# Kernel optimization log

Measured on AMD Instinct MI355X. Metric: run time of the kernel, lower is better.

## Reference

```python
import jax, jax.numpy as jnp
import numpy as np


def _ce(logits, labels):
    # per-element cross entropy; logits [N,C], labels [N] int
    logp = jax.nn.log_softmax(logits, axis=-1)
    return -jnp.take_along_axis(logp, labels[:, None].astype(jnp.int32), axis=1)[:, 0]


def _masked_mean(x, m):
    cnt = jnp.sum(m)
    return jnp.where(cnt > 0, jnp.sum(x * m) / jnp.maximum(cnt, 1.0), 0.0)


def _ohem(predict, target, train_mask, negative_ratio=3.0):
    # predict [N,2], target/train_mask [N] int {0,1}
    pos = (target * train_mask) > 0
    neg = ((1 - target) * train_mask) > 0
    n_pos = jnp.sum(pos).astype(jnp.float32)
    loss_all = _ce(predict, target)
    loss_pos = jnp.where(n_pos > 0, jnp.sum(jnp.where(pos, loss_all, 0.0)), 0.0)
    n_neg_total = jnp.sum(neg)
    n_neg = jnp.where(n_pos > 0,
                      jnp.minimum(n_neg_total, (negative_ratio * n_pos).astype(jnp.int32)),
                      jnp.minimum(100, n_neg_total))
    # hard-negative mining: top-n_neg of the per-pixel negative CE losses
    neg_sorted = jnp.sort(jnp.where(neg, loss_all, -jnp.inf))[::-1]
    loss_neg = jnp.sum(jnp.where(jnp.arange(neg_sorted.shape[0]) < n_neg, neg_sorted, 0.0))
    return (loss_pos + loss_neg) / (n_pos + n_neg.astype(jnp.float32))


def _forward(inputs, gcn_pred, gcn_labels, train_mask, tr_mask, tcl_mask, radii_map, sin_map, cos_map):
    B, C, H, W = inputs.shape
    ch = jnp.transpose(inputs, (0, 2, 3, 1)).reshape(-1, C)  # [N,8], N=B*H*W
    tr_pred = ch[:, 0:2]
    tcl_pred = ch[:, 2:4]
    sin_pred = ch[:, 4]
    cos_pred = ch[:, 5]
    scale = jnp.sqrt(1.0 / (sin_pred ** 2 + cos_pred ** 2 + 1e-4))
    sin_pred = sin_pred * scale
    cos_pred = cos_pred * scale
    top_pred = ch[:, 6]
    bot_pred = ch[:, 7]

    tm = train_mask.reshape(-1)
    tr = tr_mask.reshape(-1)
    tcl = tcl_mask[:, :, :, 0].reshape(-1)
    sin_t = sin_map.reshape(-1)
    cos_t = cos_map.reshape(-1)
    top_t = radii_map[:, :, :, 0].reshape(-1)
    bot_t = radii_map[:, :, :, 1].reshape(-1)

    # TR loss with OHEM hard-negative mining
    loss_tr = _ohem(tr_pred, tr, tm)

    # TCL loss: mean CE over train_mask*tr_mask positives
    tr_train = ((tm * tr) > 0).astype(jnp.float32)
    loss_tcl = _masked_mean(_ce(tcl_pred, tcl), tr_train)

    # geometry losses over tcl_mask pixels
    tclm = (tcl > 0).astype(jnp.float32)
    d_top = jnp.abs(top_pred / (top_t + 0.01) - 1.0)
    d_bot = jnp.abs(bot_pred / (bot_t + 0.01) - 1.0)
    sl_top = jnp.where(d_top < 1.0, 0.5 * d_top * d_top, d_top - 0.5)  # torch smooth_l1 (beta=1)
    sl_bot = jnp.where(d_bot < 1.0, 0.5 * d_bot * d_bot, d_bot - 0.5)
    loss_radii = _masked_mean(sl_top + sl_bot, tclm)

    sigma = 9.0
    d_sin = jnp.abs(sin_pred - sin_t)
    d_cos = jnp.abs(cos_pred - cos_t)
    sl_sin = jnp.where(d_sin < 1.0 / sigma, 0.5 * d_sin * d_sin * sigma, d_sin - 0.5 / sigma)
    sl_cos = jnp.where(d_cos < 1.0 / sigma, 0.5 * d_cos * d_cos * sigma, d_cos - 0.5 / sigma)
    loss_sin = _masked_mean(sl_sin, tclm)
    loss_cos = _masked_mean(sl_cos, tclm)

    gcn_loss = jnp.mean(_ce(gcn_pred, gcn_labels.reshape(-1)))
    return (loss_tr, loss_tcl, loss_sin, loss_cos, loss_radii, gcn_loss)


def setup_inputs() -> dict:
    key = jax.random.key(0)
    ks = jax.random.split(key, 9)
    B, H, W = 8, 640, 640
    return {
        'inputs': jax.random.normal(ks[0], (B, 8, H, W), dtype=jnp.float32),
        'gcn_pred': jax.random.normal(ks[1], (4096, 2), dtype=jnp.float32),
        'gcn_labels': jax.random.randint(ks[2], (4096,), 0, 2, dtype=jnp.int32),
        'train_mask': jax.random.randint(ks[3], (B, H, W), 0, 2, dtype=jnp.int32),
        'tr_mask': jax.random.randint(ks[4], (B, H, W), 0, 2, dtype=jnp.int32),
        'tcl_mask': jax.random.randint(ks[5], (B, H, W, 2), 0, 2, dtype=jnp.int32),
        'radii_map': jax.random.uniform(ks[6], (B, H, W, 2), dtype=jnp.float32),
        'sin_map': jax.random.normal(ks[7], (B, H, W), dtype=jnp.float32),
        'cos_map': jax.random.normal(ks[8], (B, H, W), dtype=jnp.float32),
    }


def reference(inputs, gcn_pred, gcn_labels, train_mask, tr_mask, tcl_mask, radii_map, sin_map, cos_map):
    return _forward(inputs, gcn_pred, gcn_labels, train_mask, tr_mask, tcl_mask, radii_map, sin_map, cos_map)
```

## Files before the change

### kernel.cpp

```cpp
#include <hip/hip_runtime.h>

#define HW_ 409600
#define NPIX 3276800
#define NB 4096
#define NGCN 4096
#define NBLK 1600

struct Ws {
  double sums[8];
  unsigned int cnts[8];
  unsigned int hcnt[NB];
  float hsum[NB];
  float pf[NBLK][8];
  unsigned int pc[NBLK][4];
};

__device__ __forceinline__ float ce2(float a0, float a1, int label) {
  float mx = fmaxf(a0, a1);
  float mn = fminf(a0, a1);
  float lse = mx + __logf(1.0f + __expf(mn - mx));
  return lse - (label ? a1 : a0);
}

struct Acc {
  float s_pos, s_neg, s_tcl, s_sin, s_cos, s_rad;
  unsigned int c_pos, c_neg, c_tcl;
  float mx_neg;
};

struct Pack {
  float4 v0, v1, v2, v3, v4, v5, v6, v7;
  int4 wtm, wtr, tca, tcb;
  float4 ra, rb, vs, vc;

  __device__ __forceinline__ void load(
      int g, const float* __restrict__ inp, const int* __restrict__ tmm,
      const int* __restrict__ trm, const int* __restrict__ tclm,
      const float* __restrict__ radm, const float* __restrict__ sinm,
      const float* __restrict__ cosm) {
    int p = g * 4;
    int b = p / HW_;
    int q = p - b * HW_;
    const float* base = inp + (size_t)b * 8 * HW_ + q;
    v0 = *(const float4*)(base);
    v1 = *(const float4*)(base + HW_);
    v2 = *(const float4*)(base + 2 * HW_);
    v3 = *(const float4*)(base + 3 * HW_);
    v4 = *(const float4*)(base + 4 * HW_);
    v5 = *(const float4*)(base + 5 * HW_);
    v6 = *(const float4*)(base + 6 * HW_);
    v7 = *(const float4*)(base + 7 * HW_);
    wtm = *(const int4*)(tmm + p);
    wtr = *(const int4*)(trm + p);
    tca = *(const int4*)(tclm + 2 * p);
    tcb = *(const int4*)(tclm + 2 * p + 4);
    ra = *(const float4*)(radm + 2 * p);
    rb = *(const float4*)(radm + 2 * p + 4);
    vs = *(const float4*)(sinm + p);
    vc = *(const float4*)(cosm + p);
  }

  __device__ __forceinline__ void compute(Acc& a) {
    float a0[4] = {v0.x, v0.y, v0.z, v0.w};
    float a1[4] = {v1.x, v1.y, v1.z, v1.w};
    float a2[4] = {v2.x, v2.y, v2.z, v2.w};
    float a3[4] = {v3.x, v3.y, v3.z, v3.w};
    float a4[4] = {v4.x, v4.y, v4.z, v4.w};
    float a5[4] = {v5.x, v5.y, v5.z, v5.w};
    float a6[4] = {v6.x, v6.y, v6.z, v6.w};
    float a7[4] = {v7.x, v7.y, v7.z, v7.w};
    int tmj[4] = {wtm.x, wtm.y, wtm.z, wtm.w};
    int trj[4] = {wtr.x, wtr.y, wtr.z, wtr.w};
    int tcj[4] = {tca.x, tca.z, tcb.x, tcb.z};
    float topt[4] = {ra.x, ra.z, rb.x, rb.z};
    float bott[4] = {ra.y, ra.w, rb.y, rb.w};
    float sint[4] = {vs.x, vs.y, vs.z, vs.w};
    float cost[4] = {vc.x, vc.y, vc.z, vc.w};
#pragma unroll
    for (int j = 0; j < 4; ++j) {
      bool pos = (trj[j] * tmj[j]) > 0;
      bool neg = ((1 - trj[j]) * tmj[j]) > 0;
      float ltr = ce2(a0[j], a1[j], trj[j]);
      if (pos) { a.s_pos += ltr; a.c_pos++; }
      if (neg) { a.s_neg += ltr; a.c_neg++; a.mx_neg = fmaxf(a.mx_neg, ltr); }
      float ltc = ce2(a2[j], a3[j], tcj[j]);
      if (pos) a.s_tcl += ltc;
      bool tc = tcj[j] > 0;
      float sp = a4[j], cp = a5[j];
      float sc = __builtin_amdgcn_rsqf(sp * sp + cp * cp + 1e-4f);
      sp *= sc; cp *= sc;
      float dsin = fabsf(sp - sint[j]);
      float dcos = fabsf(cp - cost[j]);
      const float inv9 = 1.f / 9.f;
      float slsin = dsin < inv9 ? 4.5f * dsin * dsin : dsin - 0.5f * inv9;
      float slcos = dcos < inv9 ? 4.5f * dcos * dcos : dcos - 0.5f * inv9;
      float dtop = fabsf(a6[j] * __builtin_amdgcn_rcpf(topt[j] + 0.01f) - 1.f);
      float dbot = fabsf(a7[j] * __builtin_amdgcn_rcpf(bott[j] + 0.01f) - 1.f);
      float sltop = dtop < 1.f ? 0.5f * dtop * dtop : dtop - 0.5f;
      float slbot = dbot < 1.f ? 0.5f * dbot * dbot : dbot - 0.5f;
      if (tc) { a.s_sin += slsin; a.s_cos += slcos; a.s_rad += sltop + slbot; a.c_tcl++; }
    }
  }
};

__global__ __launch_bounds__(256, 4) void k_main(
    const float* __restrict__ inp,
    const float* __restrict__ gcn_pred,
    const int* __restrict__ gcn_lab,
    const int* __restrict__ tmm,
    const int* __restrict__ trm,
    const int* __restrict__ tclm,
    const float* __restrict__ radm,
    const float* __restrict__ sinm,
    const float* __restrict__ cosm,
    Ws* __restrict__ ws) {
  Acc a = {0.f, 0.f, 0.f, 0.f, 0.f, 0.f, 0u, 0u, 0u, 0.f};
  float s_gcn = 0.f;

  int tid = threadIdx.x + blockIdx.x * blockDim.x;

  if (tid < NGCN) {
    s_gcn = ce2(gcn_pred[2 * tid], gcn_pred[2 * tid + 1], gcn_lab[tid]);
  }

  Pack A, B;
  A.load(tid,          inp, tmm, trm, tclm, radm, sinm, cosm);
  B.load(tid + 409600, inp, tmm, trm, tclm, radm, sinm, cosm);
  A.compute(a);
  B.compute(a);

#pragma unroll
  for (int off = 32; off > 0; off >>= 1) {
    a.s_pos += __shfl_down(a.s_pos, off);
    a.s_neg += __shfl_down(a.s_neg, off);
    a.s_tcl += __shfl_down(a.s_tcl, off);
    a.s_sin += __shfl_down(a.s_sin, off);
    a.s_cos += __shfl_down(a.s_cos, off);
    a.s_rad += __shfl_down(a.s_rad, off);
    s_gcn   += __shfl_down(s_gcn, off);
    a.c_pos += __shfl_down(a.c_pos, off);
    a.c_neg += __shfl_down(a.c_neg, off);
    a.c_tcl += __shfl_down(a.c_tcl, off);
    a.mx_neg = fmaxf(a.mx_neg, __shfl_down(a.mx_neg, off));
  }
  __shared__ float shf[4][8];
  __shared__ unsigned int shc[4][3];
  int wv = threadIdx.x >> 6, ln = threadIdx.x & 63;
  if (ln == 0) {
    shf[wv][0] = a.s_pos; shf[wv][1] = a.s_neg; shf[wv][2] = a.s_tcl; shf[wv][3] = a.s_sin;
    shf[wv][4] = a.s_cos; shf[wv][5] = a.s_rad; shf[wv][6] = s_gcn;  shf[wv][7] = a.mx_neg;
    shc[wv][0] = a.c_pos; shc[wv][1] = a.c_neg; shc[wv][2] = a.c_tcl;
  }
  __syncthreads();
  if (threadIdx.x == 0) {
    float f0 = 0, f1 = 0, f2 = 0, f3 = 0, f4 = 0, f5 = 0, f6 = 0, f7 = 0;
    unsigned int u0 = 0, u1 = 0, u2 = 0;
#pragma unroll
    for (int w = 0; w < 4; ++w) {
      f0 += shf[w][0]; f1 += shf[w][1]; f2 += shf[w][2]; f3 += shf[w][3];
      f4 += shf[w][4]; f5 += shf[w][5]; f6 += shf[w][6];
      f7 = fmaxf(f7, shf[w][7]);
      u0 += shc[w][0]; u1 += shc[w][1]; u2 += shc[w][2];
    }
    ws->pf[blockIdx.x][0] = f0; ws->pf[blockIdx.x][1] = f1;
    ws->pf[blockIdx.x][2] = f2; ws->pf[blockIdx.x][3] = f3;
    ws->pf[blockIdx.x][4] = f4; ws->pf[blockIdx.x][5] = f5;
    ws->pf[blockIdx.x][6] = f6; ws->pf[blockIdx.x][7] = f7;
    ws->pc[blockIdx.x][0] = u0; ws->pc[blockIdx.x][1] = u1; ws->pc[blockIdx.x][2] = u2;
  }
}

__global__ __launch_bounds__(1024) void k_reduce(Ws* __restrict__ ws, float* __restrict__ out) {
  int t = threadIdx.x;
#pragma unroll
  for (int i = t; i < NB; i += 1024) { ws->hcnt[i] = 0u; ws->hsum[i] = 0.f; }

  float f[8] = {0, 0, 0, 0, 0, 0, 0, 0};
  unsigned int u[3] = {0, 0, 0};
#pragma unroll
  for (int rep = 0; rep < 2; ++rep) {
    int s = t + rep * 1024;
    if (s < NBLK) {
#pragma unroll
      for (int i = 0; i < 7; ++i) f[i] += ws->pf[s][i];
      f[7] = fmaxf(f[7], ws->pf[s][7]);
#pragma unroll
      for (int i = 0; i < 3; ++i) u[i] += ws->pc[s][i];
    }
  }
#pragma unroll
  for (int off = 32; off > 0; off >>= 1) {
#pragma unroll
    for (int i = 0; i < 7; ++i) f[i] += __shfl_down(f[i], off);
    f[7] = fmaxf(f[7], __shfl_down(f[7], off));
#pragma unroll
    for (int i = 0; i < 3; ++i) u[i] += __shfl_down(u[i], off);
  }
  __shared__ float shf[16][8];
  __shared__ unsigned int shc[16][3];
  int wv = t >> 6, ln = t & 63;
  if (ln == 0) {
#pragma unroll
    for (int i = 0; i < 8; ++i) shf[wv][i] = f[i];
#pragma unroll
    for (int i = 0; i < 3; ++i) shc[wv][i] = u[i];
  }
  __syncthreads();
  if (t == 0) {
    double d[7] = {0, 0, 0, 0, 0, 0, 0};
    float mx = 0.f;
    unsigned int np = 0, nnt = 0, ntc = 0;
#pragma unroll
    for (int w = 0; w < 16; ++w) {
#pragma unroll
      for (int i = 0; i < 7; ++i) d[i] += (double)shf[w][i];
      mx = fmaxf(mx, shf[w][7]);
      np += shc[w][0]; nnt += shc[w][1]; ntc += shc[w][2];
    }
    ws->sums[0] = d[0];
    ws->cnts[0] = np;
    ws->cnts[5] = __float_as_uint(mx);
    out[1] = np > 0 ? (float)(d[2] / (double)np) : 0.f;
    out[2] = ntc > 0 ? (float)(d[3] / (double)ntc) : 0.f;
    out[3] = ntc > 0 ? (float)(d[4] / (double)ntc) : 0.f;
    out[4] = ntc > 0 ? (float)(d[5] / (double)ntc) : 0.f;
    out[5] = (float)(d[6] / (double)NGCN);
    long long nneg;
    if (np > 0) {
      long long cap = (long long)(int)(3.0f * (float)np);
      nneg = (long long)nnt < cap ? (long long)nnt : cap;
    } else {
      nneg = (long long)nnt < 100 ? (long long)nnt : 100;
    }
    if (nneg >= (long long)nnt) {
      out[0] = (float)((d[0] + d[1]) / ((double)np + (double)nneg));
      ws->cnts[3] = 0u;
    } else {
      ws->cnts[3] = 1u;
      ws->cnts[4] = (unsigned int)nneg;
    }
  }
}

__global__ __launch_bounds__(256) void k_hist(
    const float* __restrict__ inp,
    const int* __restrict__ tmm,
    const int* __restrict__ trm,
    Ws* __restrict__ ws) {
  if (ws->cnts[3] == 0u) return;
  __shared__ unsigned int lc[NB];
  __shared__ float lsum[NB];
  for (int i = threadIdx.x; i < NB; i += blockDim.x) { lc[i] = 0u; lsum[i] = 0.f; }
  __syncthreads();
  float maxneg = __uint_as_float(ws->cnts[5]);
  float invmax = maxneg > 0.f ? (float)NB / maxneg : 0.f;
  int tid = threadIdx.x + blockIdx.x * blockDim.x;
  int nth = blockDim.x * gridDim.x;
  for (int p = tid; p < NPIX; p += nth) {
    int tmj = tmm[p], trj = trm[p];
    if (((1 - trj) * tmj) > 0) {
      int b = p / HW_;
      int q = p - b * HW_;
      const float* base = inp + (size_t)b * 8 * HW_ + q;
      float ltr = ce2(base[0], base[HW_], trj);
      int bin = (int)(ltr * invmax);
      bin = bin < NB - 1 ? bin : NB - 1;
      bin = bin > 0 ? bin : 0;
      atomicAdd(&lc[bin], 1u);
      atomicAdd(&lsum[bin], ltr);
    }
  }
  __syncthreads();
  for (int i = threadIdx.x; i < NB; i += blockDim.x) {
    if (lc[i]) {
      atomicAdd(&ws->hcnt[i], lc[i]);
      atomicAdd(&ws->hsum[i], lsum[i]);
    }
  }
}

__global__ void k_fin2(Ws* __restrict__ ws, float* __restrict__ out) {
  if (threadIdx.x != 0 || blockIdx.x != 0) return;
  if (ws->cnts[3] == 0u) return;
  unsigned int k = ws->cnts[4];
  double acc = 0.0;
  unsigned int cum = 0;
  for (int b = NB - 1; b >= 0 && cum < k; --b) {
    unsigned int c = ws->hcnt[b];
    if (!c) continue;
    float s = ws->hsum[b];
    if (cum + c <= k) {
      acc += (double)s;
      cum += c;
    } else {
      unsigned int r = k - cum;
      acc += (double)r * ((double)s / (double)c);
      cum = k;
    }
  }
  unsigned int np = ws->cnts[0];
  double spos = ws->sums[0];
  out[0] = (float)((spos + acc) / ((double)np + (double)k));
}

extern "C" void kernel_launch(void* const* d_in, const int* in_sizes, int n_in,
                              void* d_out, int out_size, void* d_ws, size_t ws_size,
                              hipStream_t stream) {
  (void)in_sizes; (void)n_in; (void)out_size; (void)ws_size;
  const float* inp = (const float*)d_in[0];
  const float* gcn_pred = (const float*)d_in[1];
  const int* gcn_lab = (const int*)d_in[2];
  const int* tmm = (const int*)d_in[3];
  const int* trm = (const int*)d_in[4];
  const int* tclm = (const int*)d_in[5];
  const float* radm = (const float*)d_in[6];
  const float* sinm = (const float*)d_in[7];
  const float* cosm = (const float*)d_in[8];
  float* out = (float*)d_out;
  Ws* ws = (Ws*)d_ws;

  k_main<<<NBLK, 256, 0, stream>>>(inp, gcn_pred, gcn_lab, tmm, trm, tclm, radm, sinm, cosm, ws);
  k_reduce<<<1, 1024, 0, stream>>>(ws, out);
  k_hist<<<256, 256, 0, stream>>>(inp, tmm, trm, ws);
  k_fin2<<<1, 64, 0, stream>>>(ws, out);
}
```

Baseline: 54.99 us.

## Interleave dual-pack loads, fold final top-k pass into histogram kernel

The main kernel now issues all loads for both pixel groups up front, interleaved, before any compute. Its occupancy hint drops from 4 to 2 blocks per SM to leave room for the extra live registers. The separate single-thread finalisation kernel is removed: the last histogram block, found with an atomic counter that is reset in the reduce kernel, now does the top-k walk. The histogram grid shrinks from 256 to 64 blocks, which saves a launch but gives each block more pixels to process in that pass.

New measurement: 48.01 us. 1.15x faster.

```diff
diff --git a/kernel.cpp b/kernel.cpp
--- a/kernel.cpp
+++ b/kernel.cpp
@@ -5,6 +5,10 @@
 #define NB 4096
 #define NGCN 4096
 #define NBLK 1600
+#define HBLK 64
+
+typedef float vf4 __attribute__((ext_vector_type(4)));
+typedef int vi4 __attribute__((ext_vector_type(4)));
 
 struct Ws {
   double sums[8];
@@ -28,82 +32,51 @@
   float mx_neg;
 };
 
-struct Pack {
-  float4 v0, v1, v2, v3, v4, v5, v6, v7;
-  int4 wtm, wtr, tca, tcb;
-  float4 ra, rb, vs, vc;
-
-  __device__ __forceinline__ void load(
-      int g, const float* __restrict__ inp, const int* __restrict__ tmm,
-      const int* __restrict__ trm, const int* __restrict__ tclm,
-      const float* __restrict__ radm, const float* __restrict__ sinm,
-      const float* __restrict__ cosm) {
-    int p = g * 4;
-    int b = p / HW_;
-    int q = p - b * HW_;
-    const float* base = inp + (size_t)b * 8 * HW_ + q;
-    v0 = *(const float4*)(base);
-    v1 = *(const float4*)(base + HW_);
-    v2 = *(const float4*)(base + 2 * HW_);
-    v3 = *(const float4*)(base + 3 * HW_);
-    v4 = *(const float4*)(base + 4 * HW_);
-    v5 = *(const float4*)(base + 5 * HW_);
-    v6 = *(const float4*)(base + 6 * HW_);
-    v7 = *(const float4*)(base + 7 * HW_);
-    wtm = *(const int4*)(tmm + p);
-    wtr = *(const int4*)(trm + p);
-    tca = *(const int4*)(tclm + 2 * p);
-    tcb = *(const int4*)(tclm + 2 * p + 4);
-    ra = *(const float4*)(radm + 2 * p);
-    rb = *(const float4*)(radm + 2 * p + 4);
-    vs = *(const float4*)(sinm + p);
-    vc = *(const float4*)(cosm + p);
-  }
-
-  __device__ __forceinline__ void compute(Acc& a) {
-    float a0[4] = {v0.x, v0.y, v0.z, v0.w};
-    float a1[4] = {v1.x, v1.y, v1.z, v1.w};
-    float a2[4] = {v2.x, v2.y, v2.z, v2.w};
-    float a3[4] = {v3.x, v3.y, v3.z, v3.w};
-    float a4[4] = {v4.x, v4.y, v4.z, v4.w};
-    float a5[4] = {v5.x, v5.y, v5.z, v5.w};
-    float a6[4] = {v6.x, v6.y, v6.z, v6.w};
-    float a7[4] = {v7.x, v7.y, v7.z, v7.w};
-    int tmj[4] = {wtm.x, wtm.y, wtm.z, wtm.w};
-    int trj[4] = {wtr.x, wtr.y, wtr.z, wtr.w};
-    int tcj[4] = {tca.x, tca.z, tcb.x, tcb.z};
-    float topt[4] = {ra.x, ra.z, rb.x, rb.z};
-    float bott[4] = {ra.y, ra.w, rb.y, rb.w};
-    float sint[4] = {vs.x, vs.y, vs.z, vs.w};
-    float cost[4] = {vc.x, vc.y, vc.z, vc.w};
-#pragma unroll
-    for (int j = 0; j < 4; ++j) {
-      bool pos = (trj[j] * tmj[j]) > 0;
-      bool neg = ((1 - trj[j]) * tmj[j]) > 0;
-      float ltr = ce2(a0[j], a1[j], trj[j]);
-      if (pos) { a.s_pos += ltr; a.c_pos++; }
-      if (neg) { a.s_neg += ltr; a.c_neg++; a.mx_neg = fmaxf(a.mx_neg, ltr); }
-      float ltc = ce2(a2[j], a3[j], tcj[j]);
-      if (pos) a.s_tcl += ltc;
-      bool tc = tcj[j] > 0;
-      float sp = a4[j], cp = a5[j];
-      float sc = __builtin_amdgcn_rsqf(sp * sp + cp * cp + 1e-4f);
-      sp *= sc; cp *= sc;
-      float dsin = fabsf(sp - sint[j]);
-      float dcos = fabsf(cp - cost[j]);
-      const float inv9 = 1.f / 9.f;
-      float slsin = dsin < inv9 ? 4.5f * dsin * dsin : dsin - 0.5f * inv9;
-      float slcos = dcos < inv9 ? 4.5f * dcos * dcos : dcos - 0.5f * inv9;
-      float dtop = fabsf(a6[j] * __builtin_amdgcn_rcpf(topt[j] + 0.01f) - 1.f);
-      float dbot = fabsf(a7[j] * __builtin_amdgcn_rcpf(bott[j] + 0.01f) - 1.f);
-      float sltop = dtop < 1.f ? 0.5f * dtop * dtop : dtop - 0.5f;
-      float slbot = dbot < 1.f ? 0.5f * dbot * dbot : dbot - 0.5f;
-      if (tc) { a.s_sin += slsin; a.s_cos += slcos; a.s_rad += sltop + slbot; a.c_tcl++; }
-    }
-  }
-};
-
-__global__ __launch_bounds__(256, 4) void k_main(
+__device__ __forceinline__ void consume4(
+    Acc& a, vf4 v0, vf4 v1, vf4 v2, vf4 v3, vf4 v4, vf4 v5, vf4 v6, vf4 v7,
+    vi4 wtm, vi4 wtr, vi4 tca, vi4 tcb, vf4 ra, vf4 rb, vf4 vs, vf4 vc) {
+  float a0[4] = {v0.x, v0.y, v0.z, v0.w};
+  float a1[4] = {v1.x, v1.y, v1.z, v1.w};
+  float a2[4] = {v2.x, v2.y, v2.z, v2.w};
+  float a3[4] = {v3.x, v3.y, v3.z, v3.w};
+  float a4[4] = {v4.x, v4.y, v4.z, v4.w};
+  float a5[4] = {v5.x, v5.y, v5.z, v5.w};
+  float a6[4] = {v6.x, v6.y, v6.z, v6.w};
+  float a7[4] = {v7.x, v7.y, v7.z, v7.w};
+  int tmj[4] = {wtm.x, wtm.y, wtm.z, wtm.w};
+  int trj[4] = {wtr.x, wtr.y, wtr.z, wtr.w};
+  int tcj[4] = {tca.x, tca.z, tcb.x, tcb.z};
+  float topt[4] = {ra.x, ra.z, rb.x, rb.z};
+  float bott[4] = {ra.y, ra.w, rb.y, rb.w};
+  float sint[4] = {vs.x, vs.y, vs.z, vs.w};
+  float cost[4] = {vc.x, vc.y, vc.z, vc.w};
+#pragma unroll
+  for (int j = 0; j < 4; ++j) {
+    bool pos = (trj[j] * tmj[j]) > 0;
+    bool neg = ((1 - trj[j]) * tmj[j]) > 0;
+    float ltr = ce2(a0[j], a1[j], trj[j]);
+    if (pos) { a.s_pos += ltr; a.c_pos++; }
+    if (neg) { a.s_neg += ltr; a.c_neg++; a.mx_neg = fmaxf(a.mx_neg, ltr); }
+    float ltc = ce2(a2[j], a3[j], tcj[j]);
+    if (pos) a.s_tcl += ltc;
+    bool tc = tcj[j] > 0;
+    float sp = a4[j], cp = a5[j];
+    float sc = __builtin_amdgcn_rsqf(sp * sp + cp * cp + 1e-4f);
+    sp *= sc; cp *= sc;
+    float dsin = fabsf(sp - sint[j]);
+    float dcos = fabsf(cp - cost[j]);
+    const float inv9 = 1.f / 9.f;
+    float slsin = dsin < inv9 ? 4.5f * dsin * dsin : dsin - 0.5f * inv9;
+    float slcos = dcos < inv9 ? 4.5f * dcos * dcos : dcos - 0.5f * inv9;
+    float dtop = fabsf(a6[j] * __builtin_amdgcn_rcpf(topt[j] + 0.01f) - 1.f);
+    float dbot = fabsf(a7[j] * __builtin_amdgcn_rcpf(bott[j] + 0.01f) - 1.f);
+    float sltop = dtop < 1.f ? 0.5f * dtop * dtop : dtop - 0.5f;
+    float slbot = dbot < 1.f ? 0.5f * dbot * dbot : dbot - 0.5f;
+    if (tc) { a.s_sin += slsin; a.s_cos += slcos; a.s_rad += sltop + slbot; a.c_tcl++; }
+  }
+}
+
+__global__ __launch_bounds__(256, 2) void k_main(
     const float* __restrict__ inp,
     const float* __restrict__ gcn_pred,
     const int* __restrict__ gcn_lab,
@@ -123,11 +96,50 @@
     s_gcn = ce2(gcn_pred[2 * tid], gcn_pred[2 * tid + 1], gcn_lab[tid]);
   }
 
-  Pack A, B;
-  A.load(tid,          inp, tmm, trm, tclm, radm, sinm, cosm);
-  B.load(tid + 409600, inp, tmm, trm, tclm, radm, sinm, cosm);
-  A.compute(a);
-  B.compute(a);
+  {
+    int p = tid * 4;
+    int b = p / HW_;
+    int q = p - b * HW_;
+    const float* baseA = inp + (size_t)b * 8 * HW_ + q;
+    const float* baseB = baseA + (size_t)4 * 8 * HW_;
+    int pB = p + NPIX / 2;
+
+    vf4 A0 = *(const vf4*)(baseA);
+    vf4 B0 = *(const vf4*)(baseB);
+    vf4 A1 = *(const vf4*)(baseA + HW_);
+    vf4 B1 = *(const vf4*)(baseB + HW_);
+    vf4 A2 = *(const vf4*)(baseA + 2 * HW_);
+    vf4 B2 = *(const vf4*)(baseB + 2 * HW_);
+    vf4 A3 = *(const vf4*)(baseA + 3 * HW_);
+    vf4 B3 = *(const vf4*)(baseB + 3 * HW_);
+    vf4 A4 = *(const vf4*)(baseA + 4 * HW_);
+    vf4 B4 = *(const vf4*)(baseB + 4 * HW_);
+    vf4 A5 = *(const vf4*)(baseA + 5 * HW_);
+    vf4 B5 = *(const vf4*)(baseB + 5 * HW_);
+    vf4 A6 = *(const vf4*)(baseA + 6 * HW_);
+    vf4 B6 = *(const vf4*)(baseB + 6 * HW_);
+    vf4 A7 = *(const vf4*)(baseA + 7 * HW_);
+    vf4 B7 = *(const vf4*)(baseB + 7 * HW_);
+    vi4 wtmA = *(const vi4*)(tmm + p);
+    vi4 wtmB = *(const vi4*)(tmm + pB);
+    vi4 wtrA = *(const vi4*)(trm + p);
+    vi4 wtrB = *(const vi4*)(trm + pB);
+    vi4 tcaA = *(const vi4*)(tclm + 2 * p);
+    vi4 tcbA = *(const vi4*)(tclm + 2 * p + 4);
+    vi4 tcaB = *(const vi4*)(tclm + 2 * pB);
+    vi4 tcbB = *(const vi4*)(tclm + 2 * pB + 4);
+    vf4 raA = *(const vf4*)(radm + 2 * p);
+    vf4 rbA = *(const vf4*)(radm + 2 * p + 4);
+    vf4 raB = *(const vf4*)(radm + 2 * pB);
+    vf4 rbB = *(const vf4*)(radm + 2 * pB + 4);
+    vf4 vsA = *(const vf4*)(sinm + p);
+    vf4 vsB = *(const vf4*)(sinm + pB);
+    vf4 vcA = *(const vf4*)(cosm + p);
+    vf4 vcB = *(const vf4*)(cosm + pB);
+
+    consume4(a, A0, A1, A2, A3, A4, A5, A6, A7, wtmA, wtrA, tcaA, tcbA, raA, rbA, vsA, vcA);
+    consume4(a, B0, B1, B2, B3, B4, B5, B6, B7, wtmB, wtrB, tcaB, tcbB, raB, rbB, vsB, vcB);
+  }
 
 #pragma unroll
   for (int off = 32; off > 0; off >>= 1) {
@@ -178,7 +190,7 @@
   float f[8] = {0, 0, 0, 0, 0, 0, 0, 0};
   unsigned int u[3] = {0, 0, 0};
 #pragma unroll
-  for (int rep = 0; rep < 2; ++rep) {
+  for (int rep = 0; rep < (NBLK + 1023) / 1024; ++rep) {
     int s = t + rep * 1024;
     if (s < NBLK) {
 #pragma unroll
@@ -220,6 +232,7 @@
     ws->sums[0] = d[0];
     ws->cnts[0] = np;
     ws->cnts[5] = __float_as_uint(mx);
+    ws->cnts[6] = 0u;
     out[1] = np > 0 ? (float)(d[2] / (double)np) : 0.f;
     out[2] = ntc > 0 ? (float)(d[3] / (double)ntc) : 0.f;
     out[3] = ntc > 0 ? (float)(d[4] / (double)ntc) : 0.f;
@@ -246,7 +259,8 @@
     const float* __restrict__ inp,
     const int* __restrict__ tmm,
     const int* __restrict__ trm,
-    Ws* __restrict__ ws) {
+    Ws* __restrict__ ws,
+    float* __restrict__ out) {
   if (ws->cnts[3] == 0u) return;
   __shared__ unsigned int lc[NB];
   __shared__ float lsum[NB];
@@ -277,30 +291,36 @@
       atomicAdd(&ws->hsum[i], lsum[i]);
     }
   }
-}
-
-__global__ void k_fin2(Ws* __restrict__ ws, float* __restrict__ out) {
-  if (threadIdx.x != 0 || blockIdx.x != 0) return;
-  if (ws->cnts[3] == 0u) return;
-  unsigned int k = ws->cnts[4];
-  double acc = 0.0;
-  unsigned int cum = 0;
-  for (int b = NB - 1; b >= 0 && cum < k; --b) {
-    unsigned int c = ws->hcnt[b];
-    if (!c) continue;
-    float s = ws->hsum[b];
-    if (cum + c <= k) {
-      acc += (double)s;
-      cum += c;
-    } else {
-      unsigned int r = k - cum;
-      acc += (double)r * ((double)s / (double)c);
-      cum = k;
-    }
-  }
-  unsigned int np = ws->cnts[0];
-  double spos = ws->sums[0];
-  out[0] = (float)((spos + acc) / ((double)np + (double)k));
+  __shared__ unsigned int last2;
+  __threadfence();
+  __syncthreads();
+  if (threadIdx.x == 0) {
+    unsigned int old = atomicAdd(&ws->cnts[6], 1u);
+    last2 = (old == HBLK - 1) ? 1u : 0u;
+  }
+  __syncthreads();
+  if (last2 && threadIdx.x == 0) {
+    __threadfence();
+    unsigned int k = ws->cnts[4];
+    double acc = 0.0;
+    unsigned int cum = 0;
+    for (int b = NB - 1; b >= 0 && cum < k; --b) {
+      unsigned int c = ws->hcnt[b];
+      if (!c) continue;
+      float s = ws->hsum[b];
+      if (cum + c <= k) {
+        acc += (double)s;
+        cum += c;
+      } else {
+        unsigned int r = k - cum;
+        acc += (double)r * ((double)s / (double)c);
+        cum = k;
+      }
+    }
+    unsigned int np = ws->cnts[0];
+    double spos = ws->sums[0];
+    out[0] = (float)((spos + acc) / ((double)np + (double)k));
+  }
 }
 
 extern "C" void kernel_launch(void* const* d_in, const int* in_sizes, int n_in,
@@ -321,6 +341,5 @@
 
   k_main<<<NBLK, 256, 0, stream>>>(inp, gcn_pred, gcn_lab, tmm, trm, tclm, radm, sinm, cosm, ws);
   k_reduce<<<1, 1024, 0, stream>>>(ws, out);
-  k_hist<<<256, 256, 0, stream>>>(inp, tmm, trm, ws);
-  k_fin2<<<1, 64, 0, stream>>>(ws, out);
-}
+  k_hist<<<HBLK, 256, 0, stream>>>(inp, tmm, trm, ws, out);
+}
```
